# Optimization experiments

Hardware: AMD Instinct MI355X
Metric: run time of the kernel (lower is better)

## Reference

```python
import jax, jax.numpy as jnp
import numpy as np

K = 5  # kernel_size hardcoded in Net
PAD = (K - 1) // 2


def _patches(x):
    # x: [B, C, H, W] -> [B, C, K*K, H, W] (zero-padded sliding windows, like nn.Unfold)
    B, C, H, W = x.shape
    xp = jnp.pad(x, ((0, 0), (0, 0), (PAD, PAD), (PAD, PAD)))
    return jnp.stack([xp[:, :, i:i + H, j:j + W]
                      for i in range(K) for j in range(K)], axis=2)


def setup_inputs() -> dict:
    key = jax.random.key(0)
    k1, k2, k3 = jax.random.split(key, 3)
    x = jax.random.uniform(k1, (16, 1, 512, 512), dtype=jnp.float32)
    noise_var = jax.random.uniform(k2, (1,), dtype=jnp.float32)
    noise_bias = jax.random.uniform(k3, (1,), dtype=jnp.float32)
    return {"x": x, "noise_var": noise_var, "noise_bias": noise_bias}


def reference(x, noise_var, noise_bias):
    p = _patches(x)                          # [B, C, 25, H, W]
    s_var = jnp.var(p, axis=2, ddof=1)       # torch.var is unbiased by default
    mid = jnp.median(p, axis=2)              # odd window -> exact middle element
    y = x - noise_var / (s_var + 1e-10) * (x - mid + noise_bias)
    return jax.nn.relu(y)
```

## Files before the change

### kernel.cpp

```cpp
#include <hip/hip_runtime.h>

#define PAD 2
#define PX 4
#define BDX 16
#define BDY 16
#define TSX (BDX * PX)
#define TSY BDY
#define LTW (TSX + 2 * PAD)
#define LTH (TSY + 2 * PAD)

#define CE(a, b) { float _lo = fminf(a, b), _hi = fmaxf(a, b); (a) = _lo; (b) = _hi; }

#define SORT5(t0, t1, t2, t3, t4) \
    CE(t0, t1) CE(t3, t4) CE(t2, t4) CE(t2, t3) CE(t0, t3) \
    CE(t0, t2) CE(t1, t4) CE(t1, t3) CE(t1, t2)

#define TOP2(t0, t1, t2, t3, t4) \
    CE(t0, t1) CE(t2, t3) CE(t1, t3) CE(t3, t4) \
    CE(t0, t1) CE(t2, t3) CE(t1, t3)

#define BOT2(t0, t1, t2, t3, t4) \
    CE(t0, t1) CE(t2, t3) CE(t0, t2) CE(t0, t4) \
    CE(t1, t2) CE(t3, t4) CE(t1, t3)

#define MED9(q0, q1, q2, q3, q4, q5, q6, q7, q8) \
    CE(q1, q2) CE(q4, q5) CE(q7, q8) \
    CE(q0, q1) CE(q3, q4) CE(q6, q7) \
    CE(q1, q2) CE(q4, q5) CE(q7, q8) \
    CE(q0, q3) CE(q5, q8) CE(q4, q7) \
    CE(q3, q6) CE(q1, q4) CE(q2, q5) \
    CE(q4, q7) CE(q4, q2) CE(q6, q4) \
    CE(q4, q2)

__global__ __launch_bounds__(256) void denoise_median5_kernel(
    const float* __restrict__ x,
    const float* __restrict__ noise_var_p,
    const float* __restrict__ noise_bias_p,
    float* __restrict__ out,
    int H, int W)
{
    __shared__ float tile[LTH][LTW];

    const float noise_var  = noise_var_p[0];
    const float noise_bias = noise_bias_p[0];

    const int b      = blockIdx.z;
    const int tile_y = blockIdx.y * TSY;
    const int tile_x = blockIdx.x * TSX;
    const int tx = threadIdx.x;
    const int ty = threadIdx.y;
    const int tid = ty * BDX + tx;

    const float* __restrict__ img = x + (size_t)b * H * W;

    for (int i = tid; i < LTH * LTW; i += BDX * BDY) {
        const int ly = i / LTW;
        const int lx = i - ly * LTW;
        const int gy = tile_y + ly - PAD;
        const int gx = tile_x + lx - PAD;
        float v = 0.0f;
        if (gy >= 0 && gy < H && gx >= 0 && gx < W)
            v = img[gy * W + gx];
        tile[ly][lx] = v;
    }
    __syncthreads();

    float c[PX + 4][5];
    #pragma unroll
    for (int r = 0; r < 5; ++r) {
        const float* rowp = &tile[ty + r][tx * PX];
        const float4 a = *(const float4*)(rowp);
        const float4 d = *(const float4*)(rowp + 4);
        c[0][r] = a.x; c[1][r] = a.y; c[2][r] = a.z; c[3][r] = a.w;
        c[4][r] = d.x; c[5][r] = d.y; c[6][r] = d.z; c[7][r] = d.w;
    }

    float center[PX];
    #pragma unroll
    for (int p = 0; p < PX; ++p) center[p] = c[p + 2][2];

    #pragma unroll
    for (int k = 0; k < PX + 4; ++k) {
        SORT5(c[k][0], c[k][1], c[k][2], c[k][3], c[k][4]);
    }

    float s[PX + 4], q[PX + 4];
    #pragma unroll
    for (int k = 0; k < PX + 4; ++k) {
        s[k] = ((c[k][0] + c[k][1]) + (c[k][2] + c[k][3])) + c[k][4];
        float qq = c[k][0] * c[k][0];
        qq = fmaf(c[k][1], c[k][1], qq);
        qq = fmaf(c[k][2], c[k][2], qq);
        qq = fmaf(c[k][3], c[k][3], qq);
        qq = fmaf(c[k][4], c[k][4], qq);
        q[k] = qq;
    }

    float sum5[PX], sq5[PX];
    sum5[0] = ((s[0] + s[1]) + (s[2] + s[3])) + s[4];
    sq5[0]  = ((q[0] + q[1]) + (q[2] + q[3])) + q[4];
    #pragma unroll
    for (int p = 1; p < PX; ++p) {
        sum5[p] = sum5[p - 1] - s[p - 1] + s[p + 4];
        sq5[p]  = sq5[p - 1]  - q[p - 1] + q[p + 4];
    }

    float4 res;
    float* resp = (float*)&res;

    #pragma unroll
    for (int p = 0; p < PX; ++p) {
        float A1, A2;
        {
            float t0 = c[p][0], t1 = c[p+1][0], t2 = c[p+2][0], t3 = c[p+3][0], t4 = c[p+4][0];
            TOP2(t0, t1, t2, t3, t4);
            A1 = t3; A2 = t4;
        }
        float B1, B2, B3;
        {
            float t0 = c[p][1], t1 = c[p+1][1], t2 = c[p+2][1], t3 = c[p+3][1], t4 = c[p+4][1];
            SORT5(t0, t1, t2, t3, t4);
            B1 = t2; B2 = t3; B3 = t4;
        }
        float C1, C2, C3;
        {
            float t0 = c[p][2], t1 = c[p+1][2], t2 = c[p+2][2], t3 = c[p+3][2], t4 = c[p+4][2];
            SORT5(t0, t1, t2, t3, t4);
            C1 = t1; C2 = t2; C3 = t3;
        }
        float D1, D2, D3;
        {
            float t0 = c[p][3], t1 = c[p+1][3], t2 = c[p+2][3], t3 = c[p+3][3], t4 = c[p+4][3];
            SORT5(t0, t1, t2, t3, t4);
            D1 = t0; D2 = t1; D3 = t2;
        }
        float E1, E2;
        {
            float t0 = c[p][4], t1 = c[p+1][4], t2 = c[p+2][4], t3 = c[p+3][4], t4 = c[p+4][4];
            BOT2(t0, t1, t2, t3, t4);
            E1 = t0; E2 = t1;
        }

        const float mn1 = fminf(B3, D3);
        const float mn2 = fminf(C3, E2);
        const float mx1 = fmaxf(B1, D1);
        const float mx2 = fmaxf(A1, C1);

        float q0 = mx2, q1 = A2, q2 = B2, q3 = C2, q4 = D2,
              q5 = E1, q6 = mx1, q7 = mn1, q8 = mn2;
        MED9(q0, q1, q2, q3, q4, q5, q6, q7, q8);
        const float mid = q4;

        const float sum = sum5[p];
        const float sq  = sq5[p];
        const float mean = sum * (1.0f / 25.0f);
        float var = (sq - sum * mean) * (1.0f / 24.0f);
        var = fmaxf(var, 0.0f);

        const float xc = center[p];
        const float r = __builtin_amdgcn_rcpf(var + 1e-10f);
        float y = xc - noise_var * r * (xc - mid + noise_bias);
        resp[p] = fmaxf(y, 0.0f);
    }

    const int gy = tile_y + ty;
    const int gx = tile_x + tx * PX;
    *(float4*)&out[((size_t)b * H + gy) * W + gx] = res;
}

extern "C" void kernel_launch(void* const* d_in, const int* in_sizes, int n_in,
                              void* d_out, int out_size, void* d_ws, size_t ws_size,
                              hipStream_t stream)
{
    const float* x  = (const float*)d_in[0];
    const float* nv = (const float*)d_in[1];
    const float* nb = (const float*)d_in[2];
    float* out = (float*)d_out;

    const int H = 512, W = 512;
    const int B = in_sizes[0] / (H * W);

    dim3 block(BDX, BDY, 1);
    dim3 grid(W / TSX, H / TSY, B);
    denoise_median5_kernel<<<grid, block, 0, stream>>>(x, nv, nb, out, H, W);
}
```

Baseline: 32.80 us.

## Compute two output rows per thread with shared column sort, drop LDS tile

Each thread now produces two vertically adjacent rows of four pixels. The four rows the two windows share are sorted once per column, and each window's extra row is merged in with an insertion network, so the column sorts and partial sums are reused. The shared-memory tile and barrier are replaced by direct unaligned vector global loads for interior blocks, with a bounds-checked scalar path for border blocks. This removes LDS traffic and synchronisation and halves the block count, but raises register pressure and relies on the cache to serve the overlapping halo loads.

```diff
diff --git a/kernel.cpp b/kernel.cpp
--- a/kernel.cpp
+++ b/kernel.cpp
@@ -2,18 +2,28 @@
 
 #define PAD 2
 #define PX 4
+#define PY 2
 #define BDX 16
 #define BDY 16
 #define TSX (BDX * PX)
-#define TSY BDY
-#define LTW (TSX + 2 * PAD)
-#define LTH (TSY + 2 * PAD)
+#define TSY (BDY * PY)
+
+typedef float float4u __attribute__((vector_size(16), aligned(4)));
 
 #define CE(a, b) { float _lo = fminf(a, b), _hi = fmaxf(a, b); (a) = _lo; (b) = _hi; }
 
 #define SORT5(t0, t1, t2, t3, t4) \
     CE(t0, t1) CE(t3, t4) CE(t2, t4) CE(t2, t3) CE(t0, t3) \
     CE(t0, t2) CE(t1, t4) CE(t1, t3) CE(t1, t2)
+
+#define SORT4(t0, t1, t2, t3) \
+    CE(t0, t1) CE(t2, t3) CE(t0, t2) CE(t1, t3) CE(t1, t2)
+
+#define INSERT5(o0, o1, o2, o3, o4, s1, s2, s3, s4, e) { \
+    float _t  = fminf(s4, e);   o4 = fmaxf(s4, e); \
+    float _t2 = fminf(s3, _t);  o3 = fmaxf(s3, _t); \
+    float _t3 = fminf(s2, _t2); o2 = fmaxf(s2, _t2); \
+    o0 = fminf(s1, _t3);        o1 = fmaxf(s1, _t3); }
 
 #define TOP2(t0, t1, t2, t3, t4) \
     CE(t0, t1) CE(t2, t3) CE(t1, t3) CE(t3, t4) \
@@ -39,8 +49,6 @@
     float* __restrict__ out,
     int H, int W)
 {
-    __shared__ float tile[LTH][LTW];
-
     const float noise_var  = noise_var_p[0];
     const float noise_bias = noise_bias_p[0];
 
@@ -49,123 +57,158 @@
     const int tile_x = blockIdx.x * TSX;
     const int tx = threadIdx.x;
     const int ty = threadIdx.y;
-    const int tid = ty * BDX + tx;
 
     const float* __restrict__ img = x + (size_t)b * H * W;
 
-    for (int i = tid; i < LTH * LTW; i += BDX * BDY) {
-        const int ly = i / LTW;
-        const int lx = i - ly * LTW;
-        const int gy = tile_y + ly - PAD;
-        const int gx = tile_x + lx - PAD;
-        float v = 0.0f;
-        if (gy >= 0 && gy < H && gx >= 0 && gx < W)
-            v = img[gy * W + gx];
-        tile[ly][lx] = v;
-    }
-    __syncthreads();
-
-    float c[PX + 4][5];
+    const int oy0 = tile_y + ty * PY;
+    const int gx0 = tile_x + tx * PX - PAD;
+
+    float c[8][6];
+
+    const bool interior = (blockIdx.x > 0) && (blockIdx.x < gridDim.x - 1) &&
+                          (blockIdx.y > 0) && (blockIdx.y < gridDim.y - 1);
+    if (interior) {
+        const float* base = img + (size_t)(oy0 - PAD) * W + gx0;
+        #pragma unroll
+        for (int r = 0; r < 6; ++r) {
+            const float* p = base + (size_t)r * W;
+            float4u a = *(const float4u*)(p);
+            float4u d = *(const float4u*)(p + 4);
+            c[0][r] = a[0]; c[1][r] = a[1]; c[2][r] = a[2]; c[3][r] = a[3];
+            c[4][r] = d[0]; c[5][r] = d[1]; c[6][r] = d[2]; c[7][r] = d[3];
+        }
+    } else {
+        #pragma unroll
+        for (int r = 0; r < 6; ++r) {
+            const int gy = oy0 - PAD + r;
+            const bool oky = ((unsigned)gy < (unsigned)H);
+            #pragma unroll
+            for (int k = 0; k < 8; ++k) {
+                const int gx = gx0 + k;
+                const bool ok = oky && ((unsigned)gx < (unsigned)W);
+                c[k][r] = ok ? img[(size_t)gy * W + gx] : 0.0f;
+            }
+        }
+    }
+
+    float centerA[PX], centerB[PX];
     #pragma unroll
-    for (int r = 0; r < 5; ++r) {
-        const float* rowp = &tile[ty + r][tx * PX];
-        const float4 a = *(const float4*)(rowp);
-        const float4 d = *(const float4*)(rowp + 4);
-        c[0][r] = a.x; c[1][r] = a.y; c[2][r] = a.z; c[3][r] = a.w;
-        c[4][r] = d.x; c[5][r] = d.y; c[6][r] = d.z; c[7][r] = d.w;
-    }
-
-    float center[PX];
+    for (int p = 0; p < PX; ++p) { centerA[p] = c[p + 2][2]; centerB[p] = c[p + 2][3]; }
+
+    float sum5A[PX], sq5A[PX], sum5B[PX], sq5B[PX];
+    {
+        float sA8[8], qA8[8], sB8[8], qB8[8];
+        #pragma unroll
+        for (int k = 0; k < 8; ++k) {
+            const float sh = (c[k][1] + c[k][2]) + (c[k][3] + c[k][4]);
+            float qh = c[k][1] * c[k][1];
+            qh = fmaf(c[k][2], c[k][2], qh);
+            qh = fmaf(c[k][3], c[k][3], qh);
+            qh = fmaf(c[k][4], c[k][4], qh);
+            sA8[k] = sh + c[k][0];  qA8[k] = fmaf(c[k][0], c[k][0], qh);
+            sB8[k] = sh + c[k][5];  qB8[k] = fmaf(c[k][5], c[k][5], qh);
+        }
+        sum5A[0] = ((sA8[0] + sA8[1]) + (sA8[2] + sA8[3])) + sA8[4];
+        sq5A[0]  = ((qA8[0] + qA8[1]) + (qA8[2] + qA8[3])) + qA8[4];
+        sum5B[0] = ((sB8[0] + sB8[1]) + (sB8[2] + sB8[3])) + sB8[4];
+        sq5B[0]  = ((qB8[0] + qB8[1]) + (qB8[2] + qB8[3])) + qB8[4];
+        #pragma unroll
+        for (int p = 1; p < PX; ++p) {
+            sum5A[p] = sum5A[p - 1] - sA8[p - 1] + sA8[p + 4];
+            sq5A[p]  = sq5A[p - 1]  - qA8[p - 1] + qA8[p + 4];
+            sum5B[p] = sum5B[p - 1] - sB8[p - 1] + sB8[p + 4];
+            sq5B[p]  = sq5B[p - 1]  - qB8[p - 1] + qB8[p + 4];
+        }
+    }
+
     #pragma unroll
-    for (int p = 0; p < PX; ++p) center[p] = c[p + 2][2];
-
-    #pragma unroll
-    for (int k = 0; k < PX + 4; ++k) {
-        SORT5(c[k][0], c[k][1], c[k][2], c[k][3], c[k][4]);
-    }
-
-    float s[PX + 4], q[PX + 4];
-    #pragma unroll
-    for (int k = 0; k < PX + 4; ++k) {
-        s[k] = ((c[k][0] + c[k][1]) + (c[k][2] + c[k][3])) + c[k][4];
-        float qq = c[k][0] * c[k][0];
-        qq = fmaf(c[k][1], c[k][1], qq);
-        qq = fmaf(c[k][2], c[k][2], qq);
-        qq = fmaf(c[k][3], c[k][3], qq);
-        qq = fmaf(c[k][4], c[k][4], qq);
-        q[k] = qq;
-    }
-
-    float sum5[PX], sq5[PX];
-    sum5[0] = ((s[0] + s[1]) + (s[2] + s[3])) + s[4];
-    sq5[0]  = ((q[0] + q[1]) + (q[2] + q[3])) + q[4];
-    #pragma unroll
-    for (int p = 1; p < PX; ++p) {
-        sum5[p] = sum5[p - 1] - s[p - 1] + s[p + 4];
-        sq5[p]  = sq5[p - 1]  - q[p - 1] + q[p + 4];
-    }
-
-    float4 res;
-    float* resp = (float*)&res;
-
-    #pragma unroll
-    for (int p = 0; p < PX; ++p) {
-        float A1, A2;
-        {
-            float t0 = c[p][0], t1 = c[p+1][0], t2 = c[p+2][0], t3 = c[p+3][0], t4 = c[p+4][0];
-            TOP2(t0, t1, t2, t3, t4);
-            A1 = t3; A2 = t4;
-        }
-        float B1, B2, B3;
-        {
-            float t0 = c[p][1], t1 = c[p+1][1], t2 = c[p+2][1], t3 = c[p+3][1], t4 = c[p+4][1];
-            SORT5(t0, t1, t2, t3, t4);
-            B1 = t2; B2 = t3; B3 = t4;
-        }
-        float C1, C2, C3;
-        {
-            float t0 = c[p][2], t1 = c[p+1][2], t2 = c[p+2][2], t3 = c[p+3][2], t4 = c[p+4][2];
-            SORT5(t0, t1, t2, t3, t4);
-            C1 = t1; C2 = t2; C3 = t3;
-        }
-        float D1, D2, D3;
-        {
-            float t0 = c[p][3], t1 = c[p+1][3], t2 = c[p+2][3], t3 = c[p+3][3], t4 = c[p+4][3];
-            SORT5(t0, t1, t2, t3, t4);
-            D1 = t0; D2 = t1; D3 = t2;
-        }
-        float E1, E2;
-        {
-            float t0 = c[p][4], t1 = c[p+1][4], t2 = c[p+2][4], t3 = c[p+3][4], t4 = c[p+4][4];
-            BOT2(t0, t1, t2, t3, t4);
-            E1 = t0; E2 = t1;
-        }
-
-        const float mn1 = fminf(B3, D3);
-        const float mn2 = fminf(C3, E2);
-        const float mx1 = fmaxf(B1, D1);
-        const float mx2 = fmaxf(A1, C1);
-
-        float q0 = mx2, q1 = A2, q2 = B2, q3 = C2, q4 = D2,
-              q5 = E1, q6 = mx1, q7 = mn1, q8 = mn2;
-        MED9(q0, q1, q2, q3, q4, q5, q6, q7, q8);
-        const float mid = q4;
-
-        const float sum = sum5[p];
-        const float sq  = sq5[p];
-        const float mean = sum * (1.0f / 25.0f);
-        float var = (sq - sum * mean) * (1.0f / 24.0f);
-        var = fmaxf(var, 0.0f);
-
-        const float xc = center[p];
-        const float r = __builtin_amdgcn_rcpf(var + 1e-10f);
-        float y = xc - noise_var * r * (xc - mid + noise_bias);
-        resp[p] = fmaxf(y, 0.0f);
-    }
-
-    const int gy = tile_y + ty;
-    const int gx = tile_x + tx * PX;
-    *(float4*)&out[((size_t)b * H + gy) * W + gx] = res;
+    for (int k = 0; k < 8; ++k) {
+        SORT4(c[k][1], c[k][2], c[k][3], c[k][4]);
+    }
+
+    float* outp = out + (size_t)b * H * W;
+
+    auto run_window = [&](const float (&col)[8][5], const float (&center)[PX],
+                          const float (&sum5)[PX], const float (&sq5)[PX]) -> float4u {
+        float4u res;
+        #pragma unroll
+        for (int p = 0; p < PX; ++p) {
+            float A1, A2;
+            {
+                float t0 = col[p][0], t1 = col[p+1][0], t2 = col[p+2][0], t3 = col[p+3][0], t4 = col[p+4][0];
+                TOP2(t0, t1, t2, t3, t4);
+                A1 = t3; A2 = t4;
+            }
+            float B1, B2, B3;
+            {
+                float t0 = col[p][1], t1 = col[p+1][1], t2 = col[p+2][1], t3 = col[p+3][1], t4 = col[p+4][1];
+                SORT5(t0, t1, t2, t3, t4);
+                B1 = t2; B2 = t3; B3 = t4;
+            }
+            float C1, C2, C3;
+            {
+                float t0 = col[p][2], t1 = col[p+1][2], t2 = col[p+2][2], t3 = col[p+3][2], t4 = col[p+4][2];
+                SORT5(t0, t1, t2, t3, t4);
+                C1 = t1; C2 = t2; C3 = t3;
+            }
+            float D1, D2, D3;
+            {
+                float t0 = col[p][3], t1 = col[p+1][3], t2 = col[p+2][3], t3 = col[p+3][3], t4 = col[p+4][3];
+                SORT5(t0, t1, t2, t3, t4);
+                D1 = t0; D2 = t1; D3 = t2;
+            }
+            float E1, E2;
+            {
+                float t0 = col[p][4], t1 = col[p+1][4], t2 = col[p+2][4], t3 = col[p+3][4], t4 = col[p+4][4];
+                BOT2(t0, t1, t2, t3, t4);
+                E1 = t0; E2 = t1;
+            }
+
+            const float mn1 = fminf(B3, D3);
+            const float mn2 = fminf(C3, E2);
+            const float mx1 = fmaxf(B1, D1);
+            const float mx2 = fmaxf(A1, C1);
+
+            float q0 = mx2, q1 = A2, q2 = B2, q3 = C2, q4 = D2,
+                  q5 = E1, q6 = mx1, q7 = mn1, q8 = mn2;
+            MED9(q0, q1, q2, q3, q4, q5, q6, q7, q8);
+            const float mid = q4;
+
+            const float sum = sum5[p];
+            const float sq  = sq5[p];
+            const float mean = sum * (1.0f / 25.0f);
+            float var = (sq - sum * mean) * (1.0f / 24.0f);
+            var = fmaxf(var, 0.0f);
+
+            const float xc = center[p];
+            const float rr = __builtin_amdgcn_rcpf(var + 1e-10f);
+            float y = xc - noise_var * rr * (xc - mid + noise_bias);
+            res[p] = fmaxf(y, 0.0f);
+        }
+        return res;
+    };
+
+    {
+        float colA[8][5];
+        #pragma unroll
+        for (int k = 0; k < 8; ++k) {
+            INSERT5(colA[k][0], colA[k][1], colA[k][2], colA[k][3], colA[k][4],
+                    c[k][1], c[k][2], c[k][3], c[k][4], c[k][0]);
+        }
+        float4u resA = run_window(colA, centerA, sum5A, sq5A);
+        *(float4u*)(outp + (size_t)oy0 * W + tile_x + tx * PX) = resA;
+    }
+
+    {
+        float colB[8][5];
+        #pragma unroll
+        for (int k = 0; k < 8; ++k) {
+            INSERT5(colB[k][0], colB[k][1], colB[k][2], colB[k][3], colB[k][4],
+                    c[k][1], c[k][2], c[k][3], c[k][4], c[k][5]);
+        }
+        float4u resB = run_window(colB, centerB, sum5B, sq5B);
+        *(float4u*)(outp + (size_t)(oy0 + 1) * W + tile_x + tx * PX) = resB;
+    }
 }
 
 extern "C" void kernel_launch(void* const* d_in, const int* in_sizes, int n_in,
```

Result: slower. 39.06 us (+19.1%).

## Use med3/min3/max3 sorting networks, vectorized interior tile loads, packed sums

Applied to the files above, without the earlier changes.

Replaces the compare-exchange sorting networks for column sorts and the partial 5-element selections with shorter sequences built on v_min3/v_max3/v_med3 inline asm. Interior blocks load the halo tile with unaligned 16-byte vector loads instead of per-element bounds-checked loads. Column sums and sums of squares are computed on vector types before being unpacked. The aim is to cut the ALU instruction count and load instruction count, at the cost of inline asm that blocks some compiler scheduling and a branch split between interior and border blocks.

```diff
diff --git a/kernel.cpp b/kernel.cpp
--- a/kernel.cpp
+++ b/kernel.cpp
@@ -8,20 +8,22 @@
 #define TSY BDY
 #define LTW (TSX + 2 * PAD)
 #define LTH (TSY + 2 * PAD)
+#define NCHUNK (LTH * LTW / 4)
+
+typedef float float4u __attribute__((vector_size(16), aligned(4)));
+typedef float v4f __attribute__((ext_vector_type(4)));
+
+__device__ __forceinline__ float min3f(float a, float b, float c) {
+    float r; asm("v_min3_f32 %0, %1, %2, %3" : "=v"(r) : "v"(a), "v"(b), "v"(c)); return r;
+}
+__device__ __forceinline__ float max3f(float a, float b, float c) {
+    float r; asm("v_max3_f32 %0, %1, %2, %3" : "=v"(r) : "v"(a), "v"(b), "v"(c)); return r;
+}
+__device__ __forceinline__ float med3f(float a, float b, float c) {
+    float r; asm("v_med3_f32 %0, %1, %2, %3" : "=v"(r) : "v"(a), "v"(b), "v"(c)); return r;
+}
 
 #define CE(a, b) { float _lo = fminf(a, b), _hi = fmaxf(a, b); (a) = _lo; (b) = _hi; }
-
-#define SORT5(t0, t1, t2, t3, t4) \
-    CE(t0, t1) CE(t3, t4) CE(t2, t4) CE(t2, t3) CE(t0, t3) \
-    CE(t0, t2) CE(t1, t4) CE(t1, t3) CE(t1, t2)
-
-#define TOP2(t0, t1, t2, t3, t4) \
-    CE(t0, t1) CE(t2, t3) CE(t1, t3) CE(t3, t4) \
-    CE(t0, t1) CE(t2, t3) CE(t1, t3)
-
-#define BOT2(t0, t1, t2, t3, t4) \
-    CE(t0, t1) CE(t2, t3) CE(t0, t2) CE(t0, t4) \
-    CE(t1, t2) CE(t3, t4) CE(t1, t3)
 
 #define MED9(q0, q1, q2, q3, q4, q5, q6, q7, q8) \
     CE(q1, q2) CE(q4, q5) CE(q7, q8) \
@@ -53,56 +55,84 @@
 
     const float* __restrict__ img = x + (size_t)b * H * W;
 
-    for (int i = tid; i < LTH * LTW; i += BDX * BDY) {
-        const int ly = i / LTW;
-        const int lx = i - ly * LTW;
-        const int gy = tile_y + ly - PAD;
-        const int gx = tile_x + lx - PAD;
-        float v = 0.0f;
-        if (gy >= 0 && gy < H && gx >= 0 && gx < W)
-            v = img[gy * W + gx];
-        tile[ly][lx] = v;
+    const bool interior = (blockIdx.x > 0) && (blockIdx.x < gridDim.x - 1) &&
+                          (blockIdx.y > 0) && (blockIdx.y < gridDim.y - 1);
+    if (interior) {
+        const float* gbase = img + (size_t)(tile_y - PAD) * W + (tile_x - PAD);
+        {
+            const int i = tid;
+            const int row = i / 17;
+            const int cc  = i - row * 17;
+            float4u v = *(const float4u*)(gbase + (size_t)row * W + cc * 4);
+            *(float4u*)&tile[row][cc * 4] = v;
+        }
+        if (tid < NCHUNK - 256) {
+            const int i = tid + 256;
+            const int row = i / 17;
+            const int cc  = i - row * 17;
+            float4u v = *(const float4u*)(gbase + (size_t)row * W + cc * 4);
+            *(float4u*)&tile[row][cc * 4] = v;
+        }
+    } else {
+        for (int i = tid; i < LTH * LTW; i += BDX * BDY) {
+            const int ly = i / LTW;
+            const int lx = i - ly * LTW;
+            const int gy = tile_y + ly - PAD;
+            const int gx = tile_x + lx - PAD;
+            float v = 0.0f;
+            if (gy >= 0 && gy < H && gx >= 0 && gx < W)
+                v = img[(size_t)gy * W + gx];
+            tile[ly][lx] = v;
+        }
     }
     __syncthreads();
 
-    float c[PX + 4][5];
+    v4f A[5], D[5];
     #pragma unroll
     for (int r = 0; r < 5; ++r) {
-        const float* rowp = &tile[ty + r][tx * PX];
-        const float4 a = *(const float4*)(rowp);
-        const float4 d = *(const float4*)(rowp + 4);
-        c[0][r] = a.x; c[1][r] = a.y; c[2][r] = a.z; c[3][r] = a.w;
-        c[4][r] = d.x; c[5][r] = d.y; c[6][r] = d.z; c[7][r] = d.w;
-    }
-
-    float center[PX];
-    #pragma unroll
-    for (int p = 0; p < PX; ++p) center[p] = c[p + 2][2];
-
-    #pragma unroll
-    for (int k = 0; k < PX + 4; ++k) {
-        SORT5(c[k][0], c[k][1], c[k][2], c[k][3], c[k][4]);
-    }
-
-    float s[PX + 4], q[PX + 4];
-    #pragma unroll
-    for (int k = 0; k < PX + 4; ++k) {
-        s[k] = ((c[k][0] + c[k][1]) + (c[k][2] + c[k][3])) + c[k][4];
-        float qq = c[k][0] * c[k][0];
-        qq = fmaf(c[k][1], c[k][1], qq);
-        qq = fmaf(c[k][2], c[k][2], qq);
-        qq = fmaf(c[k][3], c[k][3], qq);
-        qq = fmaf(c[k][4], c[k][4], qq);
-        q[k] = qq;
-    }
+        A[r] = *(const v4f*)&tile[ty + r][tx * PX];
+        D[r] = *(const v4f*)&tile[ty + r][tx * PX + 4];
+    }
+
+    v4f SA = ((A[0] + A[1]) + (A[2] + A[3])) + A[4];
+    v4f SD = ((D[0] + D[1]) + (D[2] + D[3])) + D[4];
+    v4f QA = A[0] * A[0];
+    v4f QD = D[0] * D[0];
+    #pragma unroll
+    for (int r = 1; r < 5; ++r) { QA = A[r] * A[r] + QA; QD = D[r] * D[r] + QD; }
+
+    const float s8[8] = {SA.x, SA.y, SA.z, SA.w, SD.x, SD.y, SD.z, SD.w};
+    const float q8[8] = {QA.x, QA.y, QA.z, QA.w, QD.x, QD.y, QD.z, QD.w};
 
     float sum5[PX], sq5[PX];
-    sum5[0] = ((s[0] + s[1]) + (s[2] + s[3])) + s[4];
-    sq5[0]  = ((q[0] + q[1]) + (q[2] + q[3])) + q[4];
+    sum5[0] = ((s8[0] + s8[1]) + (s8[2] + s8[3])) + s8[4];
+    sq5[0]  = ((q8[0] + q8[1]) + (q8[2] + q8[3])) + q8[4];
     #pragma unroll
     for (int p = 1; p < PX; ++p) {
-        sum5[p] = sum5[p - 1] - s[p - 1] + s[p + 4];
-        sq5[p]  = sq5[p - 1]  - q[p - 1] + q[p + 4];
+        sum5[p] = sum5[p - 1] - s8[p - 1] + s8[p + 4];
+        sq5[p]  = sq5[p - 1]  - q8[p - 1] + q8[p + 4];
+    }
+
+    const float center[PX] = {A[2].z, A[2].w, D[2].x, D[2].y};
+
+    float c[8][5];
+    #pragma unroll
+    for (int r = 0; r < 5; ++r) {
+        c[0][r] = A[r].x; c[1][r] = A[r].y; c[2][r] = A[r].z; c[3][r] = A[r].w;
+        c[4][r] = D[r].x; c[5][r] = D[r].y; c[6][r] = D[r].z; c[7][r] = D[r].w;
+    }
+    #pragma unroll
+    for (int k = 0; k < 8; ++k) {
+        const float a1 = fminf(c[k][0], c[k][1]), a2 = fmaxf(c[k][0], c[k][1]);
+        const float b1 = fminf(c[k][2], c[k][3]), b2 = fmaxf(c[k][2], c[k][3]);
+        const float cc = c[k][4];
+        const float t1 = fminf(a2, b2), t3 = fmaxf(a1, b1);
+        const float M  = fmaxf(a2, b2), m  = fminf(a1, b1);
+        c[k][0] = fminf(m, cc);
+        c[k][4] = fmaxf(M, cc);
+        c[k][2] = med3f(t1, t3, cc);
+        c[k][3] = max3f(t1, fminf(cc, M), t3);
+        c[k][1] = min3f(t3, fmaxf(cc, m), t1);
     }
 
     float4 res;
@@ -110,35 +140,50 @@
 
     #pragma unroll
     for (int p = 0; p < PX; ++p) {
-        float A1, A2;
-        {
-            float t0 = c[p][0], t1 = c[p+1][0], t2 = c[p+2][0], t3 = c[p+3][0], t4 = c[p+4][0];
-            TOP2(t0, t1, t2, t3, t4);
-            A1 = t3; A2 = t4;
-        }
-        float B1, B2, B3;
-        {
-            float t0 = c[p][1], t1 = c[p+1][1], t2 = c[p+2][1], t3 = c[p+3][1], t4 = c[p+4][1];
-            SORT5(t0, t1, t2, t3, t4);
-            B1 = t2; B2 = t3; B3 = t4;
-        }
-        float C1, C2, C3;
-        {
-            float t0 = c[p][2], t1 = c[p+1][2], t2 = c[p+2][2], t3 = c[p+3][2], t4 = c[p+4][2];
-            SORT5(t0, t1, t2, t3, t4);
-            C1 = t1; C2 = t2; C3 = t3;
-        }
-        float D1, D2, D3;
-        {
-            float t0 = c[p][3], t1 = c[p+1][3], t2 = c[p+2][3], t3 = c[p+3][3], t4 = c[p+4][3];
-            SORT5(t0, t1, t2, t3, t4);
-            D1 = t0; D2 = t1; D3 = t2;
-        }
-        float E1, E2;
-        {
-            float t0 = c[p][4], t1 = c[p+1][4], t2 = c[p+2][4], t3 = c[p+3][4], t4 = c[p+4][4];
-            BOT2(t0, t1, t2, t3, t4);
-            E1 = t0; E2 = t1;
+        float A1, A2, B1, B2, B3, C1, C2, C3, D1, D2, D3, E1, E2;
+        {
+            const float a1 = fminf(c[p][0], c[p+1][0]), a2 = fmaxf(c[p][0], c[p+1][0]);
+            const float b1 = fminf(c[p+2][0], c[p+3][0]), b2 = fmaxf(c[p+2][0], c[p+3][0]);
+            const float cc = c[p+4][0];
+            const float M = fmaxf(a2, b2), t1 = fminf(a2, b2), t3 = fmaxf(a1, b1);
+            A2 = fmaxf(M, cc);
+            A1 = max3f(t1, fminf(cc, M), t3);
+        }
+        {
+            const float a1 = fminf(c[p][1], c[p+1][1]), a2 = fmaxf(c[p][1], c[p+1][1]);
+            const float b1 = fminf(c[p+2][1], c[p+3][1]), b2 = fmaxf(c[p+2][1], c[p+3][1]);
+            const float cc = c[p+4][1];
+            const float M = fmaxf(a2, b2), t1 = fminf(a2, b2), t3 = fmaxf(a1, b1);
+            B3 = fmaxf(M, cc);
+            B2 = max3f(t1, fminf(cc, M), t3);
+            B1 = med3f(t1, t3, cc);
+        }
+        {
+            const float a1 = fminf(c[p][2], c[p+1][2]), a2 = fmaxf(c[p][2], c[p+1][2]);
+            const float b1 = fminf(c[p+2][2], c[p+3][2]), b2 = fmaxf(c[p+2][2], c[p+3][2]);
+            const float cc = c[p+4][2];
+            const float M = fmaxf(a2, b2), m = fminf(a1, b1);
+            const float t1 = fminf(a2, b2), t3 = fmaxf(a1, b1);
+            C2 = med3f(t1, t3, cc);
+            C3 = max3f(t1, fminf(cc, M), t3);
+            C1 = min3f(t3, fmaxf(cc, m), t1);
+        }
+        {
+            const float a1 = fminf(c[p][3], c[p+1][3]), a2 = fmaxf(c[p][3], c[p+1][3]);
+            const float b1 = fminf(c[p+2][3], c[p+3][3]), b2 = fmaxf(c[p+2][3], c[p+3][3]);
+            const float cc = c[p+4][3];
+            const float m = fminf(a1, b1), t1 = fminf(a2, b2), t3 = fmaxf(a1, b1);
+            D1 = fminf(m, cc);
+            D2 = min3f(t3, fmaxf(cc, m), t1);
+            D3 = med3f(t1, t3, cc);
+        }
+        {
+            const float a1 = fminf(c[p][4], c[p+1][4]), a2 = fmaxf(c[p][4], c[p+1][4]);
+            const float b1 = fminf(c[p+2][4], c[p+3][4]), b2 = fmaxf(c[p+2][4], c[p+3][4]);
+            const float cc = c[p+4][4];
+            const float m = fminf(a1, b1), t1 = fminf(a2, b2), t3 = fmaxf(a1, b1);
+            E1 = fminf(m, cc);
+            E2 = min3f(t3, fmaxf(cc, m), t1);
         }
 
         const float mn1 = fminf(B3, D3);
@@ -158,8 +203,8 @@
         var = fmaxf(var, 0.0f);
 
         const float xc = center[p];
-        const float r = __builtin_amdgcn_rcpf(var + 1e-10f);
-        float y = xc - noise_var * r * (xc - mid + noise_bias);
+        const float rr = __builtin_amdgcn_rcpf(var + 1e-10f);
+        float y = xc - noise_var * rr * (xc - mid + noise_bias);
         resp[p] = fmaxf(y, 0.0f);
     }
 
```

New measurement: 31.65 us, median of 2. 3.5% less time.
